# Kernel tuning notes

Hardware: AMD Instinct MI355X
Metric: run time of the kernel (lower is better)

Reference implementation:

```python
import jax, jax.numpy as jnp
import numpy as np

N_TAPS = 5
N_DELAY = 1
N_ITER = 2
REF_MIC = 0
EPS = 1e-3        # eps passed to ISS updates / divisions
MODEL_EPS = 1e-5  # LaplaceModel internal eps
PB_EPS = 1e-6     # projection_back eps


def _mag_sq(x):
    return jnp.real(x) ** 2 + jnp.imag(x) ** 2


def _div(num, den, eps=EPS):
    # torchiva divide: num / clamp(den, min=eps); den is real
    return num / jnp.maximum(den, eps)


def _laplace_model(Y):
    # Laplace source model: per-source/per-frame weight 1/(2*||y(:,n)||), broadcast over freq
    denom = 2.0 * jnp.sqrt(jnp.sum(_mag_sq(Y), axis=-2, keepdims=True))
    return jnp.broadcast_to(1.0 / jnp.maximum(denom, MODEL_EPS), Y.shape)


def _demix_derev(X, X_bar, W, H):
    reverb = jnp.einsum('...cfdt,...dftn->...cfn', H, X_bar)
    sep = jnp.einsum('...cfd,...dfn->...cfn', W, X)
    return sep - reverb


def _background_update(W, H, C_XX, C_XbarX):
    n_src = W.shape[-3]
    A = (jnp.einsum('...sfc,...cfd->...fsd', W, C_XX)
         + jnp.einsum('...sfdt,...dtfc->...fsc', H, C_XbarX))
    J_H = jnp.linalg.solve(A[..., :n_src], A[..., n_src:])  # (..., f, s, c-s)
    return jnp.moveaxis(jnp.conj(J_H), -1, -3)              # (..., c-s, f, s)


def _demix_background(X, J):
    n_src = J.shape[-1]
    return jnp.einsum('...cfd,...dfn->...cfn', J, X[..., :n_src, :, :]) - X[..., n_src:, :, :]


def _iss_v1(src, X, weights, eps=EPS):
    n_frames = X.shape[-1]
    Xs = X[..., src, :, :]
    v_num = jnp.einsum('...cfn,...cfn,...fn->...cf', weights, X, jnp.conj(Xs)) / n_frames
    v_den = jnp.einsum('...cfn,...fn->...cf', weights, _mag_sq(Xs)) / n_frames
    v = _div(v_num, v_den, eps)
    v_s = 1.0 - 1.0 / jnp.sqrt(jnp.maximum(v_den[..., src, :], eps))
    return v.at[..., src, :].set(v_s.astype(v.dtype))


def _iss_v23(X, Zs, weights, eps=EPS):
    v_num = jnp.einsum('...cfn,...cfn,...fn->...cf', weights, X, jnp.conj(Zs))
    v_den = jnp.einsum('...cfn,...fn->...cf', weights, _mag_sq(Zs))
    return _div(v_num, v_den, eps)


def _iss_updates_with_H(X, X_bar, W, H, weights, J=None, Z=None, eps=EPS):
    n_src = X.shape[-3]
    n_chan = n_src if J is None else n_src + Z.shape[-3]
    n_taps = X_bar.shape[-2]
    # sequential rank-1 source updates (loop-carried; small fixed trip count)
    for src in range(n_src):
        v = _iss_v1(src, X, weights, eps)
        X = X - jnp.einsum('...cf,...fn->...cfn', v, X[..., src, :, :])
        W = W - jnp.einsum('...cf,...fd->...cfd', v, W[..., src, :, :])
        H = H - jnp.einsum('...cf,...fdt->...cfdt', v, H[..., src, :, :, :])
    if Z is not None and J is not None:
        for bak in range(n_chan - n_src):
            v = _iss_v23(X, Z[..., bak, :, :], weights, eps)
            X = X - jnp.einsum('...cf,...fn->...cfn', v, Z[..., bak, :, :])
            W = W.at[..., :n_src].add(-jnp.einsum('...cf,...fd->...cfd', v, J[..., bak, :, :]))
            W = W.at[..., n_src + bak].add(v)
    for src in range(n_chan):
        for tap in range(n_taps):
            Xst = X_bar[..., src, :, tap, :]
            v = _iss_v23(X, Xst, weights, eps)
            X = X - jnp.einsum('...cf,...fn->...cfn', v, Xst)
            H = H.at[..., src, tap].add(v)
    return X, W, H


def _one_iter(Y, X, X_bar, C_XX, C_XbarX, W, H, J, eps=EPS):
    weights = _laplace_model(Y)
    g = jnp.maximum(jnp.mean(_mag_sq(Y), axis=(-2, -1), keepdims=True), eps)
    g_sqrt = jnp.sqrt(g)
    Y = _div(Y, g_sqrt, eps)
    W = _div(W, g_sqrt, eps)
    H = _div(H, g_sqrt[..., None], eps)
    weights = weights * g
    J = _background_update(W, H, C_XX, C_XbarX)
    Z = _demix_background(X, J)
    Y, W, H = _iss_updates_with_H(Y, X_bar, W, H, weights, J=J, Z=Z, eps=eps)
    return Y, W, H, J


def _projection_back(Y, W, J, ref_mic=REF_MIC, eps=PB_EPS):
    # overdetermined branch (n_src < n_chan), ref_mic < n_src
    n_src = Y.shape[-3]
    eye = jnp.eye(n_src, dtype=W.dtype)
    W1, W2 = W[..., :n_src], W[..., n_src:]
    B = jnp.einsum('...sfc,...cfk->...sfk', W2, J) + W1  # (..., s, f, s)
    rhs = eye[:, ref_mic:ref_mic + 1]                    # (s, 1)
    BT = jnp.einsum('...sfc->...fcs', B)                 # (..., f, s, s)
    rhs_b = jnp.broadcast_to(rhs, BT.shape[:-2] + rhs.shape)
    a = jnp.linalg.solve(BT + eps * eye, rhs_b)          # (..., f, s, 1)
    a = jnp.swapaxes(a, -3, -2)                          # (..., s, f, 1)
    return Y * a


def _forward(X, n_src):
    n_chan, n_freq, n_frames = X.shape[-3:]
    batch = X.shape[:-3]
    # delayed copies: X_bar[..., c, f, t, n] = X_pad[..., c, f, n + t]
    X_pad = jnp.pad(X, [(0, 0)] * (X.ndim - 1) + [(N_TAPS + N_DELAY, 0)])
    X_bar = jnp.stack([X_pad[..., t:t + n_frames] for t in range(N_TAPS)], axis=-2)
    C_XX = jnp.einsum('...cfn,...dfn->...cfd', X, jnp.conj(X)) / n_frames
    C_XbarX = jnp.einsum('...dftn,...cfn->...dtfc', X_bar, jnp.conj(X)) / n_frames
    eye = jnp.eye(n_chan, dtype=X.dtype)[:n_src]
    W = jnp.broadcast_to(eye[:, None, :], batch + (n_src, n_freq, n_chan))
    H = jnp.zeros(batch + (n_src, n_freq, n_chan, N_TAPS), dtype=X.dtype)
    J = jnp.zeros(batch + (n_chan - n_src, n_freq, n_src), dtype=X.dtype)
    Y = X[..., :n_src, :, :]
    for _ in range(N_ITER):
        Y, W, H, J = _one_iter(Y, X, X_bar, C_XX, C_XbarX, W, H, J)
    J = _background_update(W, H, C_XX, C_XbarX)
    Y = _demix_derev(X, X_bar, W, H)
    Y = _projection_back(Y, W, J)
    return Y


def setup_inputs():
    key = jax.random.key(0)
    k1, k2 = jax.random.split(key)
    B, n_chan, n_freq, n_frames = 2, 6, 257, 1000
    X_real = jax.random.normal(k1, (B, n_chan, n_freq, n_frames), dtype=jnp.float32)
    X_imag = jax.random.normal(k2, (B, n_chan, n_freq, n_frames), dtype=jnp.float32)
    return {"X_real": X_real, "X_imag": X_imag, "n_src": 2}


def reference(X_real, X_imag, n_src):
    X = jax.lax.complex(X_real, X_imag)
    Y = _forward(X, n_src)  # (B, n_src, n_freq, n_frames) complex
    # real view of the complex output: last axis = (real, imag)
    return jnp.stack([jnp.real(Y), jnp.imag(Y)], axis=-1)
```

## Files before the change

kernel.cpp:

```cpp
#include <hip/hip_runtime.h>
#include <math.h>

#define F_   257
#define N_   1000
#define C_   6
#define S_   2
#define K_   4
#define T_   5
#define DLY  6
#define EPSF 1e-3f
#define MODEL_EPSF 1e-5f
#define PB_EPSD 1e-6
#define NTHR 512

__device__ __forceinline__ float2 cmul(float2 a, float2 b){
  return make_float2(a.x*b.x - a.y*b.y, a.x*b.y + a.y*b.x);
}
__device__ __forceinline__ float2 cadd(float2 a, float2 b){ return make_float2(a.x+b.x, a.y+b.y); }
__device__ __forceinline__ float2 csub(float2 a, float2 b){ return make_float2(a.x-b.x, a.y-b.y); }

struct dc { double x, y; };
__device__ __forceinline__ dc dmul(dc a, dc b){ return dc{a.x*b.x - a.y*b.y, a.x*b.y + a.y*b.x}; }
__device__ __forceinline__ dc dadd(dc a, dc b){ return dc{a.x+b.x, a.y+b.y}; }
__device__ __forceinline__ dc dsub(dc a, dc b){ return dc{a.x-b.x, a.y-b.y}; }
__device__ __forceinline__ dc ddiv(dc a, dc b){
  double d = b.x*b.x + b.y*b.y;
  return dc{(a.x*b.x + a.y*b.y)/d, (a.y*b.x - a.x*b.y)/d};
}
__device__ __forceinline__ dc d_of(float2 a){ return dc{(double)a.x, (double)a.y}; }

struct V2 { float2 v0, v1; };

__global__ __launch_bounds__(128) void k_weights_x(const float* __restrict__ Xre,
    const float* __restrict__ Xim, float* __restrict__ deng, float* __restrict__ gsumg)
{
  __shared__ float redw[2];
  int blk = blockIdx.x;
  int fc = blk & 15; int ch = (blk >> 4) & 7; int s = (blk >> 7) & 1; int b = blk >> 8;
  int tid = threadIdx.x;
  int n = ch*125 + tid;
  int f0 = fc*17, f1 = (f0 + 17 < F_) ? f0 + 17 : F_;
  float acc = 0.f;
  if (tid < 125){
    for (int f = f0; f < f1; ++f){
      size_t gi = ((size_t)(b*C_+s)*F_ + f)*N_ + n;
      float xr = Xre[gi], xi = Xim[gi];
      acc += xr*xr + xi*xi;
    }
    atomicAdd(&deng[(b*S_+s)*N_ + n], acc);
  }
  float r = (tid < 125) ? acc : 0.f;
  #pragma unroll
  for (int off = 32; off; off >>= 1) r += __shfl_xor(r, off);
  if ((tid & 63) == 0) redw[tid >> 6] = r;
  __syncthreads();
  if (tid == 0) atomicAdd(&gsumg[b*S_+s], redw[0] + redw[1]);
}

__global__ __launch_bounds__(128) void k_weights_y(const float2* __restrict__ Yg,
    float* __restrict__ deng, float* __restrict__ gsumg)
{
  __shared__ float redw[2];
  int blk = blockIdx.x;
  int fc = blk & 15; int ch = (blk >> 4) & 7; int s = (blk >> 7) & 1; int b = blk >> 8;
  int tid = threadIdx.x;
  int n = ch*125 + tid;
  int f0 = fc*17, f1 = (f0 + 17 < F_) ? f0 + 17 : F_;
  float acc = 0.f;
  if (tid < 125){
    for (int f = f0; f < f1; ++f){
      float2 y = Yg[(((size_t)(b*F_+f))*S_ + s)*N_ + n];
      acc += y.x*y.x + y.y*y.y;
    }
    atomicAdd(&deng[(b*S_+s)*N_ + n], acc);
  }
  float r = (tid < 125) ? acc : 0.f;
  #pragma unroll
  for (int off = 32; off; off >>= 1) r += __shfl_xor(r, off);
  if ((tid & 63) == 0) redw[tid >> 6] = r;
  __syncthreads();
  if (tid == 0) atomicAdd(&gsumg[b*S_+s], redw[0] + redw[1]);
}

__device__ __forceinline__ void bg_update(int tid, const float2* Wl,
    const float2* Hl, float2* Al, float2* Jl,
    const float2* cx, const float2* cb)
{
  if (tid < S_*C_){
    int s = tid / C_, j = tid - s*C_;
    float2 a = make_float2(0.f, 0.f);
    #pragma unroll
    for (int i = 0; i < C_; ++i) a = cadd(a, cmul(Wl[s*C_+i], cx[i*C_+j]));
    #pragma unroll
    for (int i = 0; i < C_; ++i)
      #pragma unroll
      for (int t = 0; t < T_; ++t)
        a = cadd(a, cmul(Hl[(s*C_+i)*T_+t], cb[(i*T_+t)*C_+j]));
    Al[s*C_+j] = a;
  }
  __syncthreads();
  if (tid == 0){
    dc M00 = d_of(Al[0]),  M01 = d_of(Al[1]);
    dc M10 = d_of(Al[C_]), M11 = d_of(Al[C_+1]);
    dc det = dsub(dmul(M00, M11), dmul(M01, M10));
    #pragma unroll
    for (int k = 0; k < K_; ++k){
      dc r0 = d_of(Al[2+k]), r1 = d_of(Al[C_+2+k]);
      dc x0 = ddiv(dsub(dmul(M11, r0), dmul(M01, r1)), det);
      dc x1 = ddiv(dsub(dmul(M00, r1), dmul(M10, r0)), det);
      Jl[k*S_+0] = make_float2((float)x0.x, (float)(-x0.y));
      Jl[k*S_+1] = make_float2((float)x1.x, (float)(-x1.y));
    }
  }
  __syncthreads();
}

template<typename FS>
__device__ __forceinline__ V2 round2(int tid, bool hasB, int rb, float* redl,
    float2& yA0, float2& yA1, float2& yB0, float2& yB1,
    float wA0, float wA1, float wB0, float wB1,
    FS sf, bool isV1, int src)
{
  float2 sA = sf(0), sB = sf(1);
  float m = sA.x*sA.x + sA.y*sA.y;
  float r0 = wA0*(yA0.x*sA.x + yA0.y*sA.y);
  float r1 = wA0*(yA0.y*sA.x - yA0.x*sA.y);
  float r2 = wA0*m;
  float r3 = wA1*(yA1.x*sA.x + yA1.y*sA.y);
  float r4 = wA1*(yA1.y*sA.x - yA1.x*sA.y);
  float r5 = wA1*m;
  if (hasB){
    float mb = sB.x*sB.x + sB.y*sB.y;
    r0 += wB0*(yB0.x*sB.x + yB0.y*sB.y);
    r1 += wB0*(yB0.y*sB.x - yB0.x*sB.y);
    r2 += wB0*mb;
    r3 += wB1*(yB1.x*sB.x + yB1.y*sB.y);
    r4 += wB1*(yB1.y*sB.x - yB1.x*sB.y);
    r5 += wB1*mb;
  }
  #pragma unroll
  for (int off = 32; off; off >>= 1){
    r0 += __shfl_xor(r0, off); r1 += __shfl_xor(r1, off);
    r2 += __shfl_xor(r2, off); r3 += __shfl_xor(r3, off);
    r4 += __shfl_xor(r4, off); r5 += __shfl_xor(r5, off);
  }
  int lane = tid & 63, wid = tid >> 6;
  if (lane == 0){
    float2* rw = (float2*)(redl + rb*64 + wid*8);
    rw[0] = make_float2(r0, r1);
    rw[1] = make_float2(r2, r3);
    rw[2] = make_float2(r4, r5);
  }
  __syncthreads();
  float pv = ((lane & 7) < 6) ? redl[rb*64 + (lane >> 3)*8 + (lane & 7)] : 0.f;
  pv += __shfl_xor(pv, 8);
  pv += __shfl_xor(pv, 16);
  pv += __shfl_xor(pv, 32);
  float t0 = __shfl(pv, 0), t1 = __shfl(pv, 1), t2 = __shfl(pv, 2);
  float t3 = __shfl(pv, 3), t4 = __shfl(pv, 4), t5 = __shfl(pv, 5);
  if (isV1){
    const float inv = 1.f/(float)N_;
    t0*=inv; t1*=inv; t2*=inv; t3*=inv; t4*=inv; t5*=inv;
  }
  float d0 = fmaxf(t2, EPSF), d1 = fmaxf(t5, EPSF);
  float2 v0 = make_float2(t0/d0, t1/d0);
  float2 v1 = make_float2(t3/d1, t4/d1);
  if (isV1){
    if (src == 0) v0 = make_float2(1.f - 1.f/sqrtf(d0), 0.f);
    else          v1 = make_float2(1.f - 1.f/sqrtf(d1), 0.f);
  }
  yA0 = csub(yA0, cmul(v0, sA)); yA1 = csub(yA1, cmul(v1, sA));
  if (hasB){ yB0 = csub(yB0, cmul(v0, sB)); yB1 = csub(yB1, cmul(v1, sB)); }
  return V2{v0, v1};
}

template<bool FIRST, bool FINAL>
__global__ __launch_bounds__(512, 6) void k_main(const float* __restrict__ Xre,
    const float* __restrict__ Xim, float2* __restrict__ Yg, float2* __restrict__ Wg,
    float2* __restrict__ Hg, float2* __restrict__ Cxxg,
    float2* __restrict__ Cbxg, const float* __restrict__ deng,
    const float* __restrict__ gsumg, float2* __restrict__ out2)
{
  __shared__ float2 Xl[C_*N_];
  __shared__ float2 Wl[S_*C_];
  __shared__ float2 Hl[S_*C_*T_];
  __shared__ float2 Jl[K_*S_];
  __shared__ float2 Al[S_*C_];
  __shared__ float  redl[2*64];
  __shared__ float2 Cxl[C_*C_];
  __shared__ float2 Cbl[C_*T_*C_];

  int p = blockIdx.x; int b = p / F_; int f = p - b*F_;
  int tid = threadIdx.x;
  const int nA = tid;
  const int nB = tid + NTHR;
  const bool hasB = (nB < N_);
  const int nBs = hasB ? nB : 0;

  for (int i = tid; i < C_*N_; i += NTHR){
    int c = i / N_, n = i - c*N_;
    size_t gi = ((size_t)(b*C_+c)*F_ + f)*N_ + n;
    Xl[i] = make_float2(Xre[gi], Xim[gi]);
  }
  if (tid < 128) redl[tid] = 0.f;

  float gv0 = fmaxf(gsumg[b*S_+0] * (1.f/((float)F_*(float)N_)), EPSF);
  float gv1 = fmaxf(gsumg[b*S_+1] * (1.f/((float)F_*(float)N_)), EPSF);
  float ig0 = 1.f / fmaxf(sqrtf(gv0), EPSF);
  float ig1 = 1.f / fmaxf(sqrtf(gv1), EPSF);

  float wA0 = gv0 / fmaxf(2.f*sqrtf(deng[(b*S_+0)*N_+nA]), MODEL_EPSF);
  float wA1 = gv1 / fmaxf(2.f*sqrtf(deng[(b*S_+1)*N_+nA]), MODEL_EPSF);
  float wB0 = 0.f, wB1 = 0.f;
  if (hasB){
    wB0 = gv0 / fmaxf(2.f*sqrtf(deng[(b*S_+0)*N_+nB]), MODEL_EPSF);
    wB1 = gv1 / fmaxf(2.f*sqrtf(deng[(b*S_+1)*N_+nB]), MODEL_EPSF);
  }

  if (FIRST){
    if (tid < S_*C_){
      int s = tid / C_, c = tid - s*C_;
      Wl[tid] = make_float2((s==c) ? (s ? ig1 : ig0) : 0.f, 0.f);
    }
    if (tid < S_*C_*T_) Hl[tid] = make_float2(0.f, 0.f);
  } else {
    if (tid < S_*C_){
      float ig = (tid / C_) ? ig1 : ig0;
      float2 w = Wg[(size_t)p*S_*C_ + tid];
      Wl[tid] = make_float2(w.x*ig, w.y*ig);
    }
    if (tid < S_*C_*T_){
      float ig = (tid / (C_*T_)) ? ig1 : ig0;
      float2 h = Hg[(size_t)p*S_*C_*T_ + tid];
      Hl[tid] = make_float2(h.x*ig, h.y*ig);
    }
  }
  __syncthreads();

  if (FIRST){
    int wid = tid >> 6, lane = tid & 63;
    const float inv_n = 1.0f / (float)N_;
    for (int e = wid; e < 216; e += 8){
      int a_ch, b_ch, lag;
      if (e < 36){ a_ch = e / 6; b_ch = e - a_ch*6; lag = 0; }
      else {
        int i2 = e - 36;
        a_ch = i2 / (T_*C_); int t = (i2 / C_) % T_; b_ch = i2 % C_;
        lag = DLY - t;
      }
      float accx = 0.f, accy = 0.f;
      for (int n = lane; n < N_; n += 64){
        if (n >= lag){
          float2 xa = Xl[a_ch*N_ + n - lag];
          float2 xb = Xl[b_ch*N_ + n];
          accx += xa.x*xb.x + xa.y*xb.y;
          accy += xa.y*xb.x - xa.x*xb.y;
        }
      }
      #pragma unroll
      for (int off = 32; off; off >>= 1){
        accx += __shfl_xor(accx, off);
        accy += __shfl_xor(accy, off);
      }
      if (lane == 0){
        float2 r = make_float2(accx*inv_n, accy*inv_n);
        if (e < 36){ Cxl[e] = r; Cxxg[(size_t)p*(C_*C_) + e] = r; }
        else { Cbl[e-36] = r; Cbxg[(size_t)p*(C_*T_*C_) + (e-36)] = r; }
      }
    }
    __syncthreads();
  }

  const float2* cx = FIRST ? (const float2*)Cxl : (const float2*)(Cxxg + (size_t)p*C_*C_);
  const float2* cb = FIRST ? (const float2*)Cbl : (const float2*)(Cbxg + (size_t)p*C_*T_*C_);

  float2 xA0 = Xl[nA], xA1 = Xl[N_+nA];
  float2 xB0 = make_float2(0.f,0.f), xB1 = make_float2(0.f,0.f);
  if (hasB){ xB0 = Xl[nB]; xB1 = Xl[N_+nB]; }

  float2 yA0, yA1, yB0 = make_float2(0.f,0.f), yB1 = make_float2(0.f,0.f);
  if (FIRST){
    yA0 = make_float2(xA0.x*ig0, xA0.y*ig0);
    yA1 = make_float2(xA1.x*ig1, xA1.y*ig1);
    if (hasB){
      yB0 = make_float2(xB0.x*ig0, xB0.y*ig0);
      yB1 = make_float2(xB1.x*ig1, xB1.y*ig1);
    }
  } else {
    float2 t0 = Yg[((size_t)p*S_+0)*N_+nA];
    float2 t1 = Yg[((size_t)p*S_+1)*N_+nA];
    yA0 = make_float2(t0.x*ig0, t0.y*ig0);
    yA1 = make_float2(t1.x*ig1, t1.y*ig1);
    if (hasB){
      float2 u0 = Yg[((size_t)p*S_+0)*N_+nB];
      float2 u1 = Yg[((size_t)p*S_+1)*N_+nB];
      yB0 = make_float2(u0.x*ig0, u0.y*ig0);
      yB1 = make_float2(u1.x*ig1, u1.y*ig1);
    }
  }

  bg_update(tid, Wl, Hl, Al, Jl, cx, cb);

  int rr = 0;

  for (int src2 = 0; src2 < S_; ++src2){
    V2 v = round2(tid, hasB, (rr++)&1, redl, yA0,yA1,yB0,yB1, wA0,wA1,wB0,wB1,
        [&](int k)->float2 {
          return (src2 == 0) ? (k ? yB0 : yA0) : (k ? yB1 : yA1);
        }, true, src2);
    if (tid < C_){
      float2 ws = Wl[src2*C_+tid];
      Wl[tid]      = csub(Wl[tid],      cmul(v.v0, ws));
      Wl[C_+tid]   = csub(Wl[C_+tid],   cmul(v.v1, ws));
    } else if (tid >= 64 && tid < 64 + C_*T_){
      int i = tid - 64;
      float2 hs = Hl[src2*C_*T_+i];
      Hl[i]        = csub(Hl[i],        cmul(v.v0, hs));
      Hl[C_*T_+i]  = csub(Hl[C_*T_+i],  cmul(v.v1, hs));
    }
  }

  for (int bak = 0; bak < K_; ++bak){
    float2 J0 = Jl[bak*S_+0], J1 = Jl[bak*S_+1];
    V2 v = round2(tid, hasB, (rr++)&1, redl, yA0,yA1,yB0,yB1, wA0,wA1,wB0,wB1,
        [&](int k)->float2 {
          float2 x0 = k ? xB0 : xA0;
          float2 x1 = k ? xB1 : xA1;
          int n = k ? nBs : nA;
          float2 z = cadd(cmul(J0, x0), cmul(J1, x1));
          return csub(z, Xl[(S_+bak)*N_ + n]);
        }, false, 0);
    if (tid < S_){
      float2 vv = tid ? v.v1 : v.v0;
      Wl[tid*C_+0]      = csub(Wl[tid*C_+0], cmul(vv, J0));
      Wl[tid*C_+1]      = csub(Wl[tid*C_+1], cmul(vv, J1));
      Wl[tid*C_+S_+bak] = cadd(Wl[tid*C_+S_+bak], vv);
    }
  }

  for (int sc = 0; sc < C_; ++sc){
    for (int tap = 0; tap < T_; ++tap){
      int lag = DLY - tap;
      V2 v = round2(tid, hasB, (rr++)&1, redl, yA0,yA1,yB0,yB1, wA0,wA1,wB0,wB1,
          [&](int k)->float2 {
            int n = (k ? nBs : nA) - lag;
            return (n >= 0) ? Xl[sc*N_ + n] : make_float2(0.f, 0.f);
          }, false, 0);
      if (tid < S_){
        int idx = (tid*C_+sc)*T_+tap;
        Hl[idx] = cadd(Hl[idx], tid ? v.v1 : v.v0);
      }
    }
  }

  __syncthreads();

  if (!FINAL){
    Yg[((size_t)p*S_+0)*N_+nA] = yA0;
    Yg[((size_t)p*S_+1)*N_+nA] = yA1;
    if (hasB){
      Yg[((size_t)p*S_+0)*N_+nB] = yB0;
      Yg[((size_t)p*S_+1)*N_+nB] = yB1;
    }
    if (tid < S_*C_)    Wg[(size_t)p*S_*C_ + tid]    = Wl[tid];
    if (tid < S_*C_*T_) Hg[(size_t)p*S_*C_*T_ + tid] = Hl[tid];
  } else {
    bg_update(tid, Wl, Hl, Al, Jl, cx, cb);

    float2 oA0 = make_float2(0.f,0.f), oA1 = oA0, oB0 = oA0, oB1 = oA0;
    #pragma unroll
    for (int d = 0; d < C_; ++d){
      float2 x = Xl[d*N_+nA];
      oA0 = cadd(oA0, cmul(Wl[d],    x));
      oA1 = cadd(oA1, cmul(Wl[C_+d], x));
    }
    #pragma unroll
    for (int t = 0; t < T_; ++t){
      int m = nA - (DLY - t);
      if (m >= 0){
        #pragma unroll
        for (int d = 0; d < C_; ++d){
          float2 x = Xl[d*N_+m];
          oA0 = csub(oA0, cmul(Hl[d*T_+t],      x));
          oA1 = csub(oA1, cmul(Hl[(C_+d)*T_+t], x));
        }
      }
    }
    if (hasB){
      #pragma unroll
      for (int d = 0; d < C_; ++d){
        float2 x = Xl[d*N_+nB];
        oB0 = cadd(oB0, cmul(Wl[d],    x));
        oB1 = cadd(oB1, cmul(Wl[C_+d], x));
      }
      #pragma unroll
      for (int t = 0; t < T_; ++t){
        int m = nB - (DLY - t);
        #pragma unroll
        for (int d = 0; d < C_; ++d){
          float2 x = Xl[d*N_+m];
          oB0 = csub(oB0, cmul(Hl[d*T_+t],      x));
          oB1 = csub(oB1, cmul(Hl[(C_+d)*T_+t], x));
        }
      }
    }

    if (tid == 0){
      dc Bm[2][2];
      #pragma unroll
      for (int s2 = 0; s2 < S_; ++s2)
        #pragma unroll
        for (int k = 0; k < S_; ++k){
          dc acc = d_of(Wl[s2*C_+k]);
          #pragma unroll
          for (int c = 0; c < K_; ++c)
            acc = dadd(acc, dmul(d_of(Wl[s2*C_+S_+c]), d_of(Jl[c*S_+k])));
          Bm[s2][k] = acc;
        }
      dc G00 = dc{Bm[0][0].x + PB_EPSD, Bm[0][0].y};
      dc G01 = Bm[1][0];
      dc G10 = Bm[0][1];
      dc G11 = dc{Bm[1][1].x + PB_EPSD, Bm[1][1].y};
      dc det = dsub(dmul(G00, G11), dmul(G01, G10));
      dc a0 = ddiv(G11, det);
      dc a1 = ddiv(dc{-G10.x, -G10.y}, det);
      Al[0] = make_float2((float)a0.x, (float)a0.y);
      Al[1] = make_float2((float)a1.x, (float)a1.y);
    }
    __syncthreads();
    float2 s0 = Al[0], s1 = Al[1];
    out2[((size_t)(b*S_+0)*F_ + f)*N_ + nA] = cmul(oA0, s0);
    out2[((size_t)(b*S_+1)*F_ + f)*N_ + nA] = cmul(oA1, s1);
    if (hasB){
      out2[((size_t)(b*S_+0)*F_ + f)*N_ + nB] = cmul(oB0, s0);
      out2[((size_t)(b*S_+1)*F_ + f)*N_ + nB] = cmul(oB1, s1);
    }
  }
}

extern "C" void kernel_launch(void* const* d_in, const int* in_sizes, int n_in,
                              void* d_out, int out_size, void* d_ws, size_t ws_size,
                              hipStream_t stream)
{
  const float* Xre = (const float*)d_in[0];
  const float* Xim = (const float*)d_in[1];
  int B = in_sizes[0] / (C_*F_*N_);
  int P = B*F_;

  float2* Yg    = (float2*)d_ws;
  float2* Wg    = Yg    + (size_t)P*S_*N_;
  float2* Hg    = Wg    + (size_t)P*S_*C_;
  float2* Cxxg  = Hg    + (size_t)P*S_*C_*T_;
  float2* Cbxg  = Cxxg  + (size_t)P*C_*C_;
  float*  deng0 = (float*)(Cbxg + (size_t)P*C_*T_*C_);
  float*  deng1 = deng0 + (size_t)B*S_*N_;
  float*  gsum0 = deng1 + (size_t)B*S_*N_;
  float*  gsum1 = gsum0 + (size_t)B*S_;
  float2* out2  = (float2*)d_out;

  size_t zeroBytes = (2*(size_t)B*S_*N_ + 2*(size_t)B*S_) * sizeof(float);
  int WG = B*S_*8*16;

  hipMemsetAsync(deng0, 0, zeroBytes, stream);
  k_weights_x<<<WG, 128, 0, stream>>>(Xre, Xim, deng0, gsum0);
  k_main<true,false><<<P, 512, 0, stream>>>(Xre, Xim, Yg, Wg, Hg, Cxxg, Cbxg,
                                            deng0, gsum0, nullptr);
  k_weights_y<<<WG, 128, 0, stream>>>(Yg, deng1, gsum1);
  k_main<false,true><<<P, 512, 0, stream>>>(Xre, Xim, Yg, Wg, Hg, Cxxg, Cbxg,
                                            deng1, gsum1, out2);
}
```

Before: 440.1 us.

## Batch sequential ISS rank-1 updates via Gram matrices and triangular recurrence

The sequential per-column ISS updates for the background and reverb taps each used to need a block-wide reduction and barrier. They are replaced by grouped updates: per group, warps compute in parallel the weighted projections of Y onto each column, the column norms, and the pairwise cross-Gram terms in double. The sequential coefficients are then recovered by a small forward-substitution recurrence, which cuts barrier rounds from roughly 34 to about 7. Y and the weights move into shared memory, and the occupancy hint drops from 6 to 4 blocks per CU. The cost is extra LDS traffic, redundant recomputation of z, double-precision accumulation, and the usual numerical risk from reordering the sums.

```diff
diff --git a/kernel.cpp b/kernel.cpp
--- a/kernel.cpp
+++ b/kernel.cpp
@@ -29,7 +29,16 @@
 }
 __device__ __forceinline__ dc d_of(float2 a){ return dc{(double)a.x, (double)a.y}; }
 
-struct V2 { float2 v0, v1; };
+__device__ __forceinline__ float wred(float v){
+  #pragma unroll
+  for (int off = 32; off; off >>= 1) v += __shfl_xor(v, off);
+  return v;
+}
+__device__ __forceinline__ double wredd(double v){
+  #pragma unroll
+  for (int off = 32; off; off >>= 1) v += __shfl_xor(v, off);
+  return v;
+}
 
 __global__ __launch_bounds__(128) void k_weights_x(const float* __restrict__ Xre,
     const float* __restrict__ Xim, float* __restrict__ deng, float* __restrict__ gsumg)
@@ -115,13 +124,15 @@
   __syncthreads();
 }
 
-template<typename FS>
-__device__ __forceinline__ V2 round2(int tid, bool hasB, int rb, float* redl,
-    float2& yA0, float2& yA1, float2& yB0, float2& yB1,
-    float wA0, float wA1, float wB0, float wB1,
-    FS sf, bool isV1, int src)
+template<int SRC>
+__device__ __forceinline__ void src_round(int tid, int lane, int wid, bool hasB,
+    int nA, int nBs, float* redl, float2* Yl, float2* Wl, float2* Hl,
+    float wA0, float wA1, float wB0, float wB1)
 {
-  float2 sA = sf(0), sB = sf(1);
+  float2 yA0 = Yl[nA], yA1 = Yl[N_+nA];
+  float2 yB0 = Yl[nBs], yB1 = Yl[N_+nBs];
+  float2 sA = (SRC==0) ? yA0 : yA1;
+  float2 sB = (SRC==0) ? yB0 : yB1;
   float m = sA.x*sA.x + sA.y*sA.y;
   float r0 = wA0*(yA0.x*sA.x + yA0.y*sA.y);
   float r1 = wA0*(yA0.y*sA.x - yA0.x*sA.y);
@@ -129,69 +140,81 @@
   float r3 = wA1*(yA1.x*sA.x + yA1.y*sA.y);
   float r4 = wA1*(yA1.y*sA.x - yA1.x*sA.y);
   float r5 = wA1*m;
-  if (hasB){
-    float mb = sB.x*sB.x + sB.y*sB.y;
-    r0 += wB0*(yB0.x*sB.x + yB0.y*sB.y);
-    r1 += wB0*(yB0.y*sB.x - yB0.x*sB.y);
-    r2 += wB0*mb;
-    r3 += wB1*(yB1.x*sB.x + yB1.y*sB.y);
-    r4 += wB1*(yB1.y*sB.x - yB1.x*sB.y);
-    r5 += wB1*mb;
-  }
+  float mb = sB.x*sB.x + sB.y*sB.y;
+  r0 += wB0*(yB0.x*sB.x + yB0.y*sB.y);
+  r1 += wB0*(yB0.y*sB.x - yB0.x*sB.y);
+  r2 += wB0*mb;
+  r3 += wB1*(yB1.x*sB.x + yB1.y*sB.y);
+  r4 += wB1*(yB1.y*sB.x - yB1.x*sB.y);
+  r5 += wB1*mb;
   #pragma unroll
   for (int off = 32; off; off >>= 1){
     r0 += __shfl_xor(r0, off); r1 += __shfl_xor(r1, off);
     r2 += __shfl_xor(r2, off); r3 += __shfl_xor(r3, off);
     r4 += __shfl_xor(r4, off); r5 += __shfl_xor(r5, off);
   }
-  int lane = tid & 63, wid = tid >> 6;
   if (lane == 0){
-    float2* rw = (float2*)(redl + rb*64 + wid*8);
+    float2* rw = (float2*)(redl + SRC*64 + wid*8);
     rw[0] = make_float2(r0, r1);
     rw[1] = make_float2(r2, r3);
     rw[2] = make_float2(r4, r5);
   }
   __syncthreads();
-  float pv = ((lane & 7) < 6) ? redl[rb*64 + (lane >> 3)*8 + (lane & 7)] : 0.f;
+  float pv = ((lane & 7) < 6) ? redl[SRC*64 + (lane >> 3)*8 + (lane & 7)] : 0.f;
   pv += __shfl_xor(pv, 8);
   pv += __shfl_xor(pv, 16);
   pv += __shfl_xor(pv, 32);
   float t0 = __shfl(pv, 0), t1 = __shfl(pv, 1), t2 = __shfl(pv, 2);
   float t3 = __shfl(pv, 3), t4 = __shfl(pv, 4), t5 = __shfl(pv, 5);
-  if (isV1){
-    const float inv = 1.f/(float)N_;
-    t0*=inv; t1*=inv; t2*=inv; t3*=inv; t4*=inv; t5*=inv;
-  }
+  const float inv = 1.f/(float)N_;
+  t0*=inv; t1*=inv; t2*=inv; t3*=inv; t4*=inv; t5*=inv;
   float d0 = fmaxf(t2, EPSF), d1 = fmaxf(t5, EPSF);
   float2 v0 = make_float2(t0/d0, t1/d0);
   float2 v1 = make_float2(t3/d1, t4/d1);
-  if (isV1){
-    if (src == 0) v0 = make_float2(1.f - 1.f/sqrtf(d0), 0.f);
-    else          v1 = make_float2(1.f - 1.f/sqrtf(d1), 0.f);
-  }
-  yA0 = csub(yA0, cmul(v0, sA)); yA1 = csub(yA1, cmul(v1, sA));
-  if (hasB){ yB0 = csub(yB0, cmul(v0, sB)); yB1 = csub(yB1, cmul(v1, sB)); }
-  return V2{v0, v1};
+  if (SRC == 0) v0 = make_float2(1.f - 1.f/sqrtf(d0), 0.f);
+  else          v1 = make_float2(1.f - 1.f/sqrtf(d1), 0.f);
+  Yl[nA]    = csub(yA0, cmul(v0, sA));
+  Yl[N_+nA] = csub(yA1, cmul(v1, sA));
+  if (hasB){
+    Yl[nBs]    = csub(yB0, cmul(v0, sB));
+    Yl[N_+nBs] = csub(yB1, cmul(v1, sB));
+  }
+  if (tid < C_){
+    float2 ws = Wl[SRC*C_+tid];
+    Wl[tid]    = csub(Wl[tid],    cmul(v0, ws));
+    Wl[C_+tid] = csub(Wl[C_+tid], cmul(v1, ws));
+  } else if (tid >= 64 && tid < 64 + C_*T_){
+    int i = tid - 64;
+    float2 hs = Hl[SRC*C_*T_+i];
+    Hl[i]       = csub(Hl[i],       cmul(v0, hs));
+    Hl[C_*T_+i] = csub(Hl[C_*T_+i], cmul(v1, hs));
+  }
 }
 
 template<bool FIRST, bool FINAL>
-__global__ __launch_bounds__(512, 6) void k_main(const float* __restrict__ Xre,
+__global__ __launch_bounds__(512, 4) void k_main(const float* __restrict__ Xre,
     const float* __restrict__ Xim, float2* __restrict__ Yg, float2* __restrict__ Wg,
     float2* __restrict__ Hg, float2* __restrict__ Cxxg,
     float2* __restrict__ Cbxg, const float* __restrict__ deng,
     const float* __restrict__ gsumg, float2* __restrict__ out2)
 {
   __shared__ float2 Xl[C_*N_];
+  __shared__ float2 Yl[S_*N_];
+  __shared__ float  wl[S_*N_];
   __shared__ float2 Wl[S_*C_];
   __shared__ float2 Hl[S_*C_*T_];
   __shared__ float2 Jl[K_*S_];
   __shared__ float2 Al[S_*C_];
   __shared__ float  redl[2*64];
+  __shared__ dc     AresD[T_][S_];
+  __shared__ double DresD[T_][S_];
+  __shared__ dc     GresD[10][S_];
   __shared__ float2 Cxl[C_*C_];
   __shared__ float2 Cbl[C_*T_*C_];
 
   int p = blockIdx.x; int b = p / F_; int f = p - b*F_;
   int tid = threadIdx.x;
+  int lane = tid & 63, wid = tid >> 6;
   const int nA = tid;
   const int nB = tid + NTHR;
   const bool hasB = (nB < N_);
@@ -212,9 +235,11 @@
   float wA0 = gv0 / fmaxf(2.f*sqrtf(deng[(b*S_+0)*N_+nA]), MODEL_EPSF);
   float wA1 = gv1 / fmaxf(2.f*sqrtf(deng[(b*S_+1)*N_+nA]), MODEL_EPSF);
   float wB0 = 0.f, wB1 = 0.f;
+  wl[nA] = wA0; wl[N_+nA] = wA1;
   if (hasB){
     wB0 = gv0 / fmaxf(2.f*sqrtf(deng[(b*S_+0)*N_+nB]), MODEL_EPSF);
     wB1 = gv1 / fmaxf(2.f*sqrtf(deng[(b*S_+1)*N_+nB]), MODEL_EPSF);
+    wl[nB] = wB0; wl[N_+nB] = wB1;
   }
 
   if (FIRST){
@@ -238,7 +263,28 @@
   __syncthreads();
 
   if (FIRST){
-    int wid = tid >> 6, lane = tid & 63;
+    float2 x0 = Xl[nA], x1 = Xl[N_+nA];
+    Yl[nA]    = make_float2(x0.x*ig0, x0.y*ig0);
+    Yl[N_+nA] = make_float2(x1.x*ig1, x1.y*ig1);
+    if (hasB){
+      float2 u0 = Xl[nB], u1 = Xl[N_+nB];
+      Yl[nB]    = make_float2(u0.x*ig0, u0.y*ig0);
+      Yl[N_+nB] = make_float2(u1.x*ig1, u1.y*ig1);
+    }
+  } else {
+    float2 t0 = Yg[((size_t)p*S_+0)*N_+nA];
+    float2 t1 = Yg[((size_t)p*S_+1)*N_+nA];
+    Yl[nA]    = make_float2(t0.x*ig0, t0.y*ig0);
+    Yl[N_+nA] = make_float2(t1.x*ig1, t1.y*ig1);
+    if (hasB){
+      float2 u0 = Yg[((size_t)p*S_+0)*N_+nB];
+      float2 u1 = Yg[((size_t)p*S_+1)*N_+nB];
+      Yl[nB]    = make_float2(u0.x*ig0, u0.y*ig0);
+      Yl[N_+nB] = make_float2(u1.x*ig1, u1.y*ig1);
+    }
+  }
+
+  if (FIRST){
     const float inv_n = 1.0f / (float)N_;
     for (int e = wid; e < 216; e += 8){
       int a_ch, b_ch, lag;
@@ -257,110 +303,239 @@
           accy += xa.y*xb.x - xa.x*xb.y;
         }
       }
-      #pragma unroll
-      for (int off = 32; off; off >>= 1){
-        accx += __shfl_xor(accx, off);
-        accy += __shfl_xor(accy, off);
-      }
+      accx = wred(accx); accy = wred(accy);
       if (lane == 0){
         float2 r = make_float2(accx*inv_n, accy*inv_n);
         if (e < 36){ Cxl[e] = r; Cxxg[(size_t)p*(C_*C_) + e] = r; }
         else { Cbl[e-36] = r; Cbxg[(size_t)p*(C_*T_*C_) + (e-36)] = r; }
       }
     }
-    __syncthreads();
-  }
+  }
+  __syncthreads();
 
   const float2* cx = FIRST ? (const float2*)Cxl : (const float2*)(Cxxg + (size_t)p*C_*C_);
   const float2* cb = FIRST ? (const float2*)Cbl : (const float2*)(Cbxg + (size_t)p*C_*T_*C_);
 
-  float2 xA0 = Xl[nA], xA1 = Xl[N_+nA];
-  float2 xB0 = make_float2(0.f,0.f), xB1 = make_float2(0.f,0.f);
-  if (hasB){ xB0 = Xl[nB]; xB1 = Xl[N_+nB]; }
-
-  float2 yA0, yA1, yB0 = make_float2(0.f,0.f), yB1 = make_float2(0.f,0.f);
-  if (FIRST){
-    yA0 = make_float2(xA0.x*ig0, xA0.y*ig0);
-    yA1 = make_float2(xA1.x*ig1, xA1.y*ig1);
+  bg_update(tid, Wl, Hl, Al, Jl, cx, cb);
+
+  src_round<0>(tid, lane, wid, hasB, nA, nBs, redl, Yl, Wl, Hl, wA0, wA1, wB0, wB1);
+  src_round<1>(tid, lane, wid, hasB, nA, nBs, redl, Yl, Wl, Hl, wA0, wA1, wB0, wB1);
+  __syncthreads();
+
+  {
+    for (int tsk = wid; tsk < 10; tsk += 8){
+      if (tsk < 4){
+        int k = tsk;
+        float2 j0 = Jl[k*S_+0], j1 = Jl[k*S_+1];
+        double ar0=0,ai0=0,ar1=0,ai1=0,dd0=0,dd1=0;
+        for (int n = lane; n < N_; n += 64){
+          float2 x0 = Xl[n], x1 = Xl[N_+n];
+          float2 z = csub(cadd(cmul(j0,x0), cmul(j1,x1)), Xl[(S_+k)*N_+n]);
+          float w0 = wl[n], w1 = wl[N_+n];
+          float2 y0 = Yl[n], y1 = Yl[N_+n];
+          ar0 += (double)(w0*(y0.x*z.x + y0.y*z.y));
+          ai0 += (double)(w0*(y0.y*z.x - y0.x*z.y));
+          ar1 += (double)(w1*(y1.x*z.x + y1.y*z.y));
+          ai1 += (double)(w1*(y1.y*z.x - y1.x*z.y));
+          float m = z.x*z.x + z.y*z.y;
+          dd0 += (double)(w0*m); dd1 += (double)(w1*m);
+        }
+        ar0=wredd(ar0); ai0=wredd(ai0); ar1=wredd(ar1); ai1=wredd(ai1);
+        dd0=wredd(dd0); dd1=wredd(dd1);
+        if (lane == 0){
+          AresD[k][0] = dc{ar0, ai0};
+          AresD[k][1] = dc{ar1, ai1};
+          DresD[k][0] = dd0; DresD[k][1] = dd1;
+        }
+      } else {
+        int q = tsk - 4;
+        int ka = (q < 3) ? 0 : (q < 5 ? 1 : 2);
+        int kb = (q < 3) ? (q + 1) : (q < 5 ? (q - 1) : 3);
+        float2 ja0=Jl[ka*S_+0], ja1=Jl[ka*S_+1];
+        float2 jb0=Jl[kb*S_+0], jb1=Jl[kb*S_+1];
+        double gr0=0,gi0=0,gr1=0,gi1=0;
+        for (int n = lane; n < N_; n += 64){
+          float2 x0 = Xl[n], x1 = Xl[N_+n];
+          float2 za = csub(cadd(cmul(ja0,x0), cmul(ja1,x1)), Xl[(S_+ka)*N_+n]);
+          float2 zb = csub(cadd(cmul(jb0,x0), cmul(jb1,x1)), Xl[(S_+kb)*N_+n]);
+          float pr = za.x*zb.x + za.y*zb.y;
+          float pi = za.y*zb.x - za.x*zb.y;
+          float w0 = wl[n], w1 = wl[N_+n];
+          gr0 += (double)(w0*pr); gi0 += (double)(w0*pi);
+          gr1 += (double)(w1*pr); gi1 += (double)(w1*pi);
+        }
+        gr0=wredd(gr0); gi0=wredd(gi0); gr1=wredd(gr1); gi1=wredd(gi1);
+        if (lane == 0){
+          GresD[q][0] = dc{gr0, gi0};
+          GresD[q][1] = dc{gr1, gi1};
+        }
+      }
+    }
+    __syncthreads();
+
+    float2 vz[K_][S_];
+    #pragma unroll
+    for (int s = 0; s < S_; ++s){
+      dc av[K_];
+      #pragma unroll
+      for (int k = 0; k < K_; ++k) av[k] = AresD[k][s];
+      #pragma unroll
+      for (int i = 0; i < K_; ++i){
+        double dd = fmax(DresD[i][s], (double)EPSF);
+        float2 v = make_float2((float)(av[i].x/dd), (float)(av[i].y/dd));
+        vz[i][s] = v;
+        dc vd = dc{(double)v.x, (double)v.y};
+        #pragma unroll
+        for (int j = i+1; j < K_; ++j){
+          const int zbase = (i==0) ? 0 : (i==1) ? 3 : 5;
+          int q = zbase + (j - i - 1);
+          av[j] = dsub(av[j], dmul(vd, GresD[q][s]));
+        }
+      }
+    }
+    {
+      float2 x0 = Xl[nA], x1 = Xl[N_+nA];
+      float2 y0 = Yl[nA], y1 = Yl[N_+nA];
+      #pragma unroll
+      for (int k = 0; k < K_; ++k){
+        float2 z = csub(cadd(cmul(Jl[k*S_+0], x0), cmul(Jl[k*S_+1], x1)), Xl[(S_+k)*N_+nA]);
+        y0 = csub(y0, cmul(vz[k][0], z));
+        y1 = csub(y1, cmul(vz[k][1], z));
+      }
+      Yl[nA] = y0; Yl[N_+nA] = y1;
+      if (hasB){
+        float2 u0 = Xl[nB], u1 = Xl[N_+nB];
+        float2 p0 = Yl[nB], p1 = Yl[N_+nB];
+        #pragma unroll
+        for (int k = 0; k < K_; ++k){
+          float2 z = csub(cadd(cmul(Jl[k*S_+0], u0), cmul(Jl[k*S_+1], u1)), Xl[(S_+k)*N_+nB]);
+          p0 = csub(p0, cmul(vz[k][0], z));
+          p1 = csub(p1, cmul(vz[k][1], z));
+        }
+        Yl[nB] = p0; Yl[N_+nB] = p1;
+      }
+    }
+    if (tid == 0){
+      #pragma unroll
+      for (int s = 0; s < S_; ++s)
+        #pragma unroll
+        for (int k = 0; k < K_; ++k){
+          Wl[s*C_+0]    = csub(Wl[s*C_+0], cmul(vz[k][s], Jl[k*S_+0]));
+          Wl[s*C_+1]    = csub(Wl[s*C_+1], cmul(vz[k][s], Jl[k*S_+1]));
+          Wl[s*C_+S_+k] = cadd(Wl[s*C_+S_+k], vz[k][s]);
+        }
+    }
+    __syncthreads();
+  }
+
+  for (int c = 0; c < C_; ++c){
+    const float2* Xc = Xl + c*N_;
+    for (int tsk = wid; tsk < 15; tsk += 8){
+      if (tsk < 5){
+        int lag = DLY - tsk;
+        double ar0=0,ai0=0,ar1=0,ai1=0,dd0=0,dd1=0;
+        for (int n = lane; n < N_; n += 64){
+          float2 x = (n >= lag) ? Xc[n-lag] : make_float2(0.f,0.f);
+          float w0 = wl[n], w1 = wl[N_+n];
+          float2 y0 = Yl[n], y1 = Yl[N_+n];
+          ar0 += (double)(w0*(y0.x*x.x + y0.y*x.y));
+          ai0 += (double)(w0*(y0.y*x.x - y0.x*x.y));
+          ar1 += (double)(w1*(y1.x*x.x + y1.y*x.y));
+          ai1 += (double)(w1*(y1.y*x.x - y1.x*x.y));
+          float m = x.x*x.x + x.y*x.y;
+          dd0 += (double)(w0*m); dd1 += (double)(w1*m);
+        }
+        ar0=wredd(ar0); ai0=wredd(ai0); ar1=wredd(ar1); ai1=wredd(ai1);
+        dd0=wredd(dd0); dd1=wredd(dd1);
+        if (lane == 0){
+          AresD[tsk][0] = dc{ar0, ai0};
+          AresD[tsk][1] = dc{ar1, ai1};
+          DresD[tsk][0] = dd0; DresD[tsk][1] = dd1;
+        }
+      } else {
+        int q = tsk - 5;
+        int ta = (q < 4) ? 0 : (q < 7) ? 1 : (q < 9) ? 2 : 3;
+        int tb = (q < 4) ? (q + 1) : (q < 7) ? (q - 2) : (q < 9) ? (q - 4) : 4;
+        int l1 = DLY - ta, l2 = DLY - tb;
+        double gr0=0,gi0=0,gr1=0,gi1=0;
+        for (int n = lane; n < N_; n += 64){
+          float2 x1 = (n >= l1) ? Xc[n-l1] : make_float2(0.f,0.f);
+          float2 x2 = (n >= l2) ? Xc[n-l2] : make_float2(0.f,0.f);
+          float pr = x1.x*x2.x + x1.y*x2.y;
+          float pi = x1.y*x2.x - x1.x*x2.y;
+          float w0 = wl[n], w1 = wl[N_+n];
+          gr0 += (double)(w0*pr); gi0 += (double)(w0*pi);
+          gr1 += (double)(w1*pr); gi1 += (double)(w1*pi);
+        }
+        gr0=wredd(gr0); gi0=wredd(gi0); gr1=wredd(gr1); gi1=wredd(gi1);
+        if (lane == 0){
+          GresD[q][0] = dc{gr0, gi0};
+          GresD[q][1] = dc{gr1, gi1};
+        }
+      }
+    }
+    __syncthreads();
+
+    float2 vt[T_][S_];
+    #pragma unroll
+    for (int s = 0; s < S_; ++s){
+      dc av[T_];
+      #pragma unroll
+      for (int t = 0; t < T_; ++t) av[t] = AresD[t][s];
+      #pragma unroll
+      for (int i = 0; i < T_; ++i){
+        double dd = fmax(DresD[i][s], (double)EPSF);
+        float2 v = make_float2((float)(av[i].x/dd), (float)(av[i].y/dd));
+        vt[i][s] = v;
+        dc vd = dc{(double)v.x, (double)v.y};
+        #pragma unroll
+        for (int j = i+1; j < T_; ++j){
+          const int base = (i==0) ? 0 : (i==1) ? 4 : (i==2) ? 7 : 9;
+          int q = base + (j - i - 1);
+          av[j] = dsub(av[j], dmul(vd, GresD[q][s]));
+        }
+      }
+    }
+    {
+      float2 y0 = Yl[nA], y1 = Yl[N_+nA];
+      #pragma unroll
+      for (int t = 0; t < T_; ++t){
+        int lag = DLY - t;
+        float2 x = (nA >= lag) ? Xc[nA-lag] : make_float2(0.f,0.f);
+        y0 = csub(y0, cmul(vt[t][0], x));
+        y1 = csub(y1, cmul(vt[t][1], x));
+      }
+      Yl[nA] = y0; Yl[N_+nA] = y1;
+      if (hasB){
+        float2 p0 = Yl[nB], p1 = Yl[N_+nB];
+        #pragma unroll
+        for (int t = 0; t < T_; ++t){
+          int lag = DLY - t;
+          float2 x = Xc[nB-lag];
+          p0 = csub(p0, cmul(vt[t][0], x));
+          p1 = csub(p1, cmul(vt[t][1], x));
+        }
+        Yl[nB] = p0; Yl[N_+nB] = p1;
+      }
+    }
+    if (tid == 0){
+      #pragma unroll
+      for (int s = 0; s < S_; ++s)
+        #pragma unroll
+        for (int t = 0; t < T_; ++t){
+          int idx = (s*C_+c)*T_+t;
+          Hl[idx] = cadd(Hl[idx], vt[t][s]);
+        }
+    }
+    __syncthreads();
+  }
+
+  if (!FINAL){
+    Yg[((size_t)p*S_+0)*N_+nA] = Yl[nA];
+    Yg[((size_t)p*S_+1)*N_+nA] = Yl[N_+nA];
     if (hasB){
-      yB0 = make_float2(xB0.x*ig0, xB0.y*ig0);
-      yB1 = make_float2(xB1.x*ig1, xB1.y*ig1);
-    }
-  } else {
-    float2 t0 = Yg[((size_t)p*S_+0)*N_+nA];
-    float2 t1 = Yg[((size_t)p*S_+1)*N_+nA];
-    yA0 = make_float2(t0.x*ig0, t0.y*ig0);
-    yA1 = make_float2(t1.x*ig1, t1.y*ig1);
-    if (hasB){
-      float2 u0 = Yg[((size_t)p*S_+0)*N_+nB];
-      float2 u1 = Yg[((size_t)p*S_+1)*N_+nB];
-      yB0 = make_float2(u0.x*ig0, u0.y*ig0);
-      yB1 = make_float2(u1.x*ig1, u1.y*ig1);
-    }
-  }
-
-  bg_update(tid, Wl, Hl, Al, Jl, cx, cb);
-
-  int rr = 0;
-
-  for (int src2 = 0; src2 < S_; ++src2){
-    V2 v = round2(tid, hasB, (rr++)&1, redl, yA0,yA1,yB0,yB1, wA0,wA1,wB0,wB1,
-        [&](int k)->float2 {
-          return (src2 == 0) ? (k ? yB0 : yA0) : (k ? yB1 : yA1);
-        }, true, src2);
-    if (tid < C_){
-      float2 ws = Wl[src2*C_+tid];
-      Wl[tid]      = csub(Wl[tid],      cmul(v.v0, ws));
-      Wl[C_+tid]   = csub(Wl[C_+tid],   cmul(v.v1, ws));
-    } else if (tid >= 64 && tid < 64 + C_*T_){
-      int i = tid - 64;
-      float2 hs = Hl[src2*C_*T_+i];
-      Hl[i]        = csub(Hl[i],        cmul(v.v0, hs));
-      Hl[C_*T_+i]  = csub(Hl[C_*T_+i],  cmul(v.v1, hs));
-    }
-  }
-
-  for (int bak = 0; bak < K_; ++bak){
-    float2 J0 = Jl[bak*S_+0], J1 = Jl[bak*S_+1];
-    V2 v = round2(tid, hasB, (rr++)&1, redl, yA0,yA1,yB0,yB1, wA0,wA1,wB0,wB1,
-        [&](int k)->float2 {
-          float2 x0 = k ? xB0 : xA0;
-          float2 x1 = k ? xB1 : xA1;
-          int n = k ? nBs : nA;
-          float2 z = cadd(cmul(J0, x0), cmul(J1, x1));
-          return csub(z, Xl[(S_+bak)*N_ + n]);
-        }, false, 0);
-    if (tid < S_){
-      float2 vv = tid ? v.v1 : v.v0;
-      Wl[tid*C_+0]      = csub(Wl[tid*C_+0], cmul(vv, J0));
-      Wl[tid*C_+1]      = csub(Wl[tid*C_+1], cmul(vv, J1));
-      Wl[tid*C_+S_+bak] = cadd(Wl[tid*C_+S_+bak], vv);
-    }
-  }
-
-  for (int sc = 0; sc < C_; ++sc){
-    for (int tap = 0; tap < T_; ++tap){
-      int lag = DLY - tap;
-      V2 v = round2(tid, hasB, (rr++)&1, redl, yA0,yA1,yB0,yB1, wA0,wA1,wB0,wB1,
-          [&](int k)->float2 {
-            int n = (k ? nBs : nA) - lag;
-            return (n >= 0) ? Xl[sc*N_ + n] : make_float2(0.f, 0.f);
-          }, false, 0);
-      if (tid < S_){
-        int idx = (tid*C_+sc)*T_+tap;
-        Hl[idx] = cadd(Hl[idx], tid ? v.v1 : v.v0);
-      }
-    }
-  }
-
-  __syncthreads();
-
-  if (!FINAL){
-    Yg[((size_t)p*S_+0)*N_+nA] = yA0;
-    Yg[((size_t)p*S_+1)*N_+nA] = yA1;
-    if (hasB){
-      Yg[((size_t)p*S_+0)*N_+nB] = yB0;
-      Yg[((size_t)p*S_+1)*N_+nB] = yB1;
+      Yg[((size_t)p*S_+0)*N_+nB] = Yl[nB];
+      Yg[((size_t)p*S_+1)*N_+nB] = Yl[N_+nB];
     }
     if (tid < S_*C_)    Wg[(size_t)p*S_*C_ + tid]    = Wl[tid];
     if (tid < S_*C_*T_) Hg[(size_t)p*S_*C_*T_ + tid] = Hl[tid];
@@ -413,8 +588,8 @@
         for (int k = 0; k < S_; ++k){
           dc acc = d_of(Wl[s2*C_+k]);
           #pragma unroll
-          for (int c = 0; c < K_; ++c)
-            acc = dadd(acc, dmul(d_of(Wl[s2*C_+S_+c]), d_of(Jl[c*S_+k])));
+          for (int cc = 0; cc < K_; ++cc)
+            acc = dadd(acc, dmul(d_of(Wl[s2*C_+S_+cc]), d_of(Jl[cc*S_+k])));
           Bm[s2][k] = acc;
         }
       dc G00 = dc{Bm[0][0].x + PB_EPSD, Bm[0][0].y};
```

Result: slower. 738.1 us (+67.7%).
